# Optimization experiments

Measured on AMD Instinct MI355X. Metric: run time of the kernel, lower is better.

Reference implementation:

```python
import jax, jax.numpy as jnp
import numpy as np

N_NODES = 100000
N_EDGES = 3200000
N_FEAT = 16
N_GRAPHS = 1024


def setup_inputs() -> dict:
    key = jax.random.key(0)
    ks = jax.random.split(key, 12)
    x = jax.random.normal(ks[0], (N_NODES, N_FEAT), dtype=jnp.float32)
    edge_index = jax.random.randint(ks[1], (2, N_EDGES), 0, N_NODES, dtype=jnp.int32)
    batch = jnp.sort(jax.random.randint(ks[2], (N_NODES,), 0, N_GRAPHS, dtype=jnp.int32))
    def lin(k, fan_in, fan_out):
        s = 1.0 / np.sqrt(fan_in)
        return jax.random.uniform(k, (fan_in, fan_out), jnp.float32, -s, s)
    W1 = lin(ks[3], N_FEAT, 64); b1 = jnp.zeros((64,), jnp.float32)
    W2 = lin(ks[4], 64, 32);     b2 = jnp.zeros((32,), jnp.float32)
    fc1_W = lin(ks[5], 32, 16);  fc1_b = jnp.zeros((16,), jnp.float32)
    fc2_W = lin(ks[6], 16, 1);   fc2_b = jnp.zeros((1,), jnp.float32)
    return {"x": x, "edge_index": edge_index, "batch": batch,
            "W1": W1, "b1": b1, "W2": W2, "b2": b2,
            "fc1_W": fc1_W, "fc1_b": fc1_b, "fc2_W": fc2_W, "fc2_b": fc2_b}


def _gcn_conv(h, W, b, src, dst, norm, n_nodes):
    # h: [N, Fin] -> [N, Fout]; symmetric-normalized scatter-add (PyG GCNConv)
    h = h @ W
    msg = h[src] * norm[:, None]            # edge-wise gather + scale
    out = jax.ops.segment_sum(msg, dst, num_segments=n_nodes)
    return out + b


def reference(x, edge_index, batch, W1, b1, W2, b2, fc1_W, fc1_b, fc2_W, fc2_b):
    n_nodes = x.shape[0]
    # add self-loops
    loops = jnp.arange(n_nodes, dtype=edge_index.dtype)
    src = jnp.concatenate([edge_index[0], loops])
    dst = jnp.concatenate([edge_index[1], loops])
    deg = jax.ops.segment_sum(jnp.ones_like(dst, dtype=x.dtype), dst, num_segments=n_nodes)
    dinv = jnp.where(deg > 0, jax.lax.rsqrt(deg), 0.0)
    norm = dinv[src] * dinv[dst]

    h = jax.nn.relu(_gcn_conv(x, W1, b1, src, dst, norm, n_nodes))
    # dropout p=0.2 is identity at inference
    h = jax.nn.relu(_gcn_conv(h, W2, b2, src, dst, norm, n_nodes))

    # global mean pool over graphs
    sums = jax.ops.segment_sum(h, batch, num_segments=N_GRAPHS)
    cnts = jax.ops.segment_sum(jnp.ones((n_nodes,), h.dtype), batch, num_segments=N_GRAPHS)
    g = sums / jnp.maximum(cnts, 1.0)[:, None]

    g = jax.nn.relu(g @ fc1_W + fc1_b)
    # dropout p=0.5 is identity at inference
    out = g @ fc2_W + fc2_b
    return jax.nn.sigmoid(out)  # [N_GRAPHS, 1]
```

## Files before the change

kernel.cpp:

```cpp
#include <hip/hip_runtime.h>
#include <math.h>

#define NNODES  100000
#define NEDGES  3200000
#define NGRAPHS 1024
#define BNODES  196
#define NBUCK   ((NNODES + BNODES - 1) / BNODES)
#define SCAP    12288
#define SLDS    7168
#define CHUNK   4096
#define NCHUNKS ((NEDGES + CHUNK - 1) / CHUNK)

typedef int iv4 __attribute__((ext_vector_type(4)));
typedef float fv2 __attribute__((ext_vector_type(2)));

#if defined(__has_builtin)
#if __has_builtin(__builtin_amdgcn_cvt_pk_f32_fp8) && __has_builtin(__builtin_amdgcn_cvt_pk_fp8_f32)
#define HW_FP8 1
#endif
#endif

__device__ __forceinline__ unsigned bf16pair(float a, float b) {
    unsigned ua = __float_as_uint(a), ub = __float_as_uint(b);
    ua += 0x7fffu + ((ua >> 16) & 1u);
    ub += 0x7fffu + ((ub >> 16) & 1u);
    return (ua >> 16) | (ub & 0xffff0000u);
}
__device__ __forceinline__ float bflo(unsigned u) { return __uint_as_float(u << 16); }
__device__ __forceinline__ float bfhi(unsigned u) { return __uint_as_float(u & 0xffff0000u); }

__device__ __forceinline__ unsigned fp8_of(float v) {
    unsigned s = (__float_as_uint(v) >> 24) & 0x80u;
    float a = fminf(fabsf(v), 448.f);
    unsigned ub = __float_as_uint(a);
    unsigned lsb = (ub >> 20) & 1u;
    ub += 0x0007FFFFu + lsb;
    int em = (int)(ub >> 20) - (120 << 3);
    if (em < 1) return s;
    if (em > 0x7E) em = 0x7E;
    return s | (unsigned)em;
}
__device__ __forceinline__ float fp8_to_f(unsigned b) {
    unsigned em = b & 0x7Fu;
    unsigned s = (b & 0x80u) << 24;
    float f = __uint_as_float(s | ((em + 0x3C0u) << 20));
    return (em >= 8u) ? f : 0.f;
}
__device__ __forceinline__ unsigned fp8x4_pack(float a, float b, float c, float d) {
    a = fminf(fmaxf(a, -448.f), 448.f);
    b = fminf(fmaxf(b, -448.f), 448.f);
    c = fminf(fmaxf(c, -448.f), 448.f);
    d = fminf(fmaxf(d, -448.f), 448.f);
#ifdef HW_FP8
    int w = __builtin_amdgcn_cvt_pk_fp8_f32(a, b, 0, false);
    w = __builtin_amdgcn_cvt_pk_fp8_f32(c, d, w, true);
    return (unsigned)w;
#else
    return fp8_of(a) | (fp8_of(b) << 8) | (fp8_of(c) << 16) | (fp8_of(d) << 24);
#endif
}
__device__ __forceinline__ fv2 f8lo(unsigned w) {
#ifdef HW_FP8
    return __builtin_amdgcn_cvt_pk_f32_fp8((int)w, false);
#else
    fv2 t; t.x = fp8_to_f(w & 0xFFu); t.y = fp8_to_f((w >> 8) & 0xFFu); return t;
#endif
}
__device__ __forceinline__ fv2 f8hi(unsigned w) {
#ifdef HW_FP8
    return __builtin_amdgcn_cvt_pk_f32_fp8((int)w, true);
#else
    fv2 t; t.x = fp8_to_f((w >> 16) & 0xFFu); t.y = fp8_to_f(w >> 24); return t;
#endif
}


__global__ void zero4_kernel(int4* p, int nvec) {
    int i = blockIdx.x * blockDim.x + threadIdx.x;
    if (i < nvec) p[i] = make_int4(0, 0, 0, 0);
}


__global__ void binA_kernel(const int* __restrict__ src, const int* __restrict__ dst,
                            int* __restrict__ bucketCur, int* __restrict__ stage) {
    __shared__ int lcnt[NBUCK + 1];
    __shared__ int boff[NBUCK + 1];
    __shared__ int gbase[NBUCK + 1];
    __shared__ int cur[NBUCK + 1];
    __shared__ int wtot[4];
    __shared__ int packed[CHUNK];
    __shared__ unsigned short bof[CHUNK];
    int tid = threadIdx.x;
    int beg = blockIdx.x * CHUNK;
    int end = beg + CHUNK; if (end > NEDGES) end = NEDGES;
    int cnt = end - beg;

    for (int i = tid; i <= NBUCK; i += 256) lcnt[i] = 0;
    __syncthreads();

    int ent[16];
    int bk[16];
#pragma unroll
    for (int it = 0; it < 4; ++it) {
        int e0 = beg + tid * 4 + it * 1024;
        if (e0 < end) {
            iv4 d4 = __builtin_nontemporal_load((const iv4*)(dst + e0));
            iv4 s4 = __builtin_nontemporal_load((const iv4*)(src + e0));
            int b;
            b = d4.x / BNODES; ent[it*4+0] = s4.x | ((d4.x - b*BNODES) << 17); bk[it*4+0] = b; atomicAdd(&lcnt[b], 1);
            b = d4.y / BNODES; ent[it*4+1] = s4.y | ((d4.y - b*BNODES) << 17); bk[it*4+1] = b; atomicAdd(&lcnt[b], 1);
            b = d4.z / BNODES; ent[it*4+2] = s4.z | ((d4.z - b*BNODES) << 17); bk[it*4+2] = b; atomicAdd(&lcnt[b], 1);
            b = d4.w / BNODES; ent[it*4+3] = s4.w | ((d4.w - b*BNODES) << 17); bk[it*4+3] = b; atomicAdd(&lcnt[b], 1);
        } else {
            bk[it*4+0] = -1; bk[it*4+1] = -1; bk[it*4+2] = -1; bk[it*4+3] = -1;
            ent[it*4+0] = 0; ent[it*4+1] = 0; ent[it*4+2] = 0; ent[it*4+3] = 0;
        }
    }
    __syncthreads();

    int b0 = 2 * tid, b1 = 2 * tid + 1;
    int c0 = lcnt[b0];
    int c1 = (b1 < NBUCK) ? lcnt[b1] : 0;
    int sum = c0 + c1;
    int lane = tid & 63, wid = tid >> 6;
    int v = sum;
#pragma unroll
    for (int o = 1; o < 64; o <<= 1) {
        int t = __shfl_up(v, o, 64);
        if (lane >= o) v += t;
    }
    if (lane == 63) wtot[wid] = v;
    __syncthreads();
    int woff = 0;
#pragma unroll
    for (int w = 0; w < 4; ++w) woff += (w < wid) ? wtot[w] : 0;
    int excl = woff + v - sum;
    boff[b0] = excl; cur[b0] = excl;
    if (b1 < NBUCK) { boff[b1] = excl + c0; cur[b1] = excl + c0; }
    if (c0 > 0) gbase[b0] = atomicAdd(&bucketCur[b0], c0);
    if (b1 < NBUCK && c1 > 0) gbase[b1] = atomicAdd(&bucketCur[b1], c1);
    __syncthreads();

#pragma unroll
    for (int k = 0; k < 16; ++k) {
        int b = bk[k];
        if (b >= 0) {
            int p = atomicAdd(&cur[b], 1);
            packed[p] = ent[k];
            bof[p] = (unsigned short)b;
        }
    }
    __syncthreads();

    for (int i = tid; i < cnt; i += 256) {
        int b = bof[i];
        int addr = b * SCAP + gbase[b] + (i - boff[b]);
        stage[addr] = packed[i];
    }
}


__global__ void scanE_kernel(const int* __restrict__ bucketCur, int* __restrict__ ebase) {
    int lane = threadIdx.x;
    int run = 0;
    for (int base = 0; base < NBUCK; base += 64) {
        int idx = base + lane;
        int own = (idx < NBUCK) ? bucketCur[idx] : 0;
        int v = own;
        for (int o = 1; o < 64; o <<= 1) {
            int t = __shfl_up(v, o, 64);
            if (lane >= o) v += t;
        }
        if (idx < NBUCK) ebase[idx] = run + v - own;
        run += __shfl(v, 63, 64);
    }
}


__global__ void binB_kernel(const int* __restrict__ bucketCur, const int* __restrict__ ebase,
                            const int* __restrict__ stage, const float2* __restrict__ x,
                            int* __restrict__ entries, int* __restrict__ rowptr,
                            float* __restrict__ dinv, unsigned* __restrict__ xs) {
    __shared__ int s[256];
    __shared__ int ncur[256];
    __shared__ float ndinv[256];
    __shared__ int wt[4];
    __shared__ int se[SLDS];
    int b = blockIdx.x;
    int cntE = bucketCur[b];
    int eb = ebase[b];
    int nlo = b * BNODES;
    int nn = NNODES - nlo; if (nn > BNODES) nn = BNODES;
    int sb = b * SCAP;
    int tid = threadIdx.x;

    s[tid] = 0;
    __syncthreads();
    for (int e = tid; e < cntE; e += 256) {
        int w = stage[sb + e];
        if (e < SLDS) se[e] = w;
        atomicAdd(&s[(unsigned)w >> 17], 1);
    }
    __syncthreads();
    int v = s[tid];
    int lane = tid & 63, wid = tid >> 6;
    int iv = v;
#pragma unroll
    for (int o = 1; o < 64; o <<= 1) {
        int t = __shfl_up(iv, o, 64);
        if (lane >= o) iv += t;
    }
    if (lane == 63) wt[wid] = iv;
    __syncthreads();
    int woff = 0;
#pragma unroll
    for (int w2 = 0; w2 < 4; ++w2) woff += (w2 < wid) ? wt[w2] : 0;
    int excl = woff + iv - v;
    ncur[tid] = excl;
    if (tid < nn) {
        rowptr[nlo + tid] = eb + excl;
        float di = rsqrtf((float)(v + 1));
        dinv[nlo + tid] = di;
        ndinv[tid] = di;
    }
    if (b == NBUCK - 1 && tid == 0) rowptr[NNODES] = NEDGES;
    __syncthreads();
    for (int i = tid; i < nn * 8; i += 256) {
        int node = i >> 3, w = i & 7;
        float2 v2 = x[(size_t)(nlo + node) * 8 + w];
        float di = ndinv[node];
        xs[(nlo + node) * 8 + w] = bf16pair(v2.x * di, v2.y * di);
    }
    for (int e = tid; e < cntE; e += 256) {
        unsigned w = (unsigned)((e < SLDS) ? se[e] : stage[sb + e]);
        int dl = (int)(w >> 17);
        int slot = atomicAdd(&ncur[dl], 1);
        entries[eb + slot] = (int)(w & 0x1FFFFu);
    }
}


__device__ __forceinline__ void acc_bf(unsigned u, fv2& a) {
    fv2 t; t.x = bflo(u); t.y = bfhi(u);
    a += t;
}
#define ACCX4(V) { acc_bf((V).x, acc0); acc_bf((V).y, acc1); acc_bf((V).z, acc2); acc_bf((V).w, acc3); }
#define QRED(a) { a.x += __shfl_xor(a.x, 2); a.y += __shfl_xor(a.y, 2); \
                  a.x += __shfl_xor(a.x, 4); a.y += __shfl_xor(a.y, 4); }

__global__ void __launch_bounds__(256) gatherX_mlp_kernel(const int* __restrict__ entries,
        const int* __restrict__ rowptr, const float* __restrict__ dinv,
        const uint4* __restrict__ xsv,
        const float* __restrict__ W1, const float* __restrict__ b1,
        const float* __restrict__ W2, unsigned* __restrict__ hm2f) {
    __shared__ __align__(16) float w1s[16 * 64];
    __shared__ __align__(16) float w2s[64 * 32];
    __shared__ float bb1[64];
    int tid = threadIdx.x;
    for (int i = tid; i < 16 * 64; i += 256) w1s[i] = W1[i];
    for (int i = tid; i < 64 * 32; i += 256) w2s[i] = W2[i];
    if (tid < 64) bb1[tid] = b1[tid];
    __syncthreads();

    int t = blockIdx.x * 256 + tid;
    int n = t >> 3, lane = t & 7;
    int half = lane & 1, quad = lane >> 1;
    int beg = rowptr[n], end = rowptr[n + 1];
    fv2 acc0 = {0.f, 0.f}, acc1 = {0.f, 0.f}, acc2 = {0.f, 0.f}, acc3 = {0.f, 0.f};
    if (quad == 0) {
        uint4 sv = xsv[n * 2 + half];
        ACCX4(sv);
    }

    int nb = (end - beg) >> 4;
    const int* ep = entries + beg + (quad << 2);
    iv4 e = {0, 0, 0, 0};
    if (nb > 0) __builtin_memcpy(&e, ep, 16);
    for (int i = 1; i <= nb; ++i) {
        iv4 f = e;
        if (i < nb) __builtin_memcpy(&e, ep + (i << 4), 16);
        uint4 v0 = xsv[f.x * 2 + half];
        uint4 v1 = xsv[f.y * 2 + half];
        uint4 v2 = xsv[f.z * 2 + half];
        uint4 v3 = xsv[f.w * 2 + half];
        ACCX4(v0); ACCX4(v1); ACCX4(v2); ACCX4(v3);
    }
    int tp = beg + (nb << 4) + (quad << 2);
#pragma unroll
    for (int j = 0; j < 4; ++j) {
        if (tp + j < end) {
            int ee = entries[tp + j];
            uint4 v = xsv[ee * 2 + half];
            ACCX4(v);
        }
    }

    QRED(acc0); QRED(acc1); QRED(acc2); QRED(acc3);

    float di = dinv[n];
    float own[8];
    own[0] = acc0.x * di; own[1] = acc0.y * di; own[2] = acc1.x * di; own[3] = acc1.y * di;
    own[4] = acc2.x * di; own[5] = acc2.y * di; own[6] = acc3.x * di; own[7] = acc3.y * di;
    float oth[8];
#pragma unroll
    for (int i2 = 0; i2 < 8; ++i2) oth[i2] = __shfl_xor(own[i2], 1);
    float a16[16];
#pragma unroll
    for (int k = 0; k < 8; ++k) a16[k]     = (half == 0) ? own[k] : oth[k];
#pragma unroll
    for (int k = 0; k < 8; ++k) a16[8 + k] = (half == 0) ? oth[k] : own[k];

    float h[8];
    {
        int j0 = lane * 8;
#pragma unroll
        for (int jj = 0; jj < 8; ++jj) h[jj] = bb1[j0 + jj];
#pragma unroll
        for (int k = 0; k < 16; ++k) {
            const float4* wr = (const float4*)(w1s + k * 64 + j0);
            float4 wa = wr[0], wb = wr[1];
            float av = a16[k];
            h[0] += av * wa.x; h[1] += av * wa.y; h[2] += av * wa.z; h[3] += av * wa.w;
            h[4] += av * wb.x; h[5] += av * wb.y; h[6] += av * wb.z; h[7] += av * wb.w;
        }
#pragma unroll
        for (int jj = 0; jj < 8; ++jj) h[jj] = fmaxf(h[jj], 0.f);
    }

    {
        int j0c = lane * 4;
        float c0 = 0.f, c1 = 0.f, c2 = 0.f, c3 = 0.f;
#pragma unroll
        for (int k = 0; k < 64; ++k) {
            float hv = __shfl(h[k & 7], k >> 3, 8);
            float4 w = *(const float4*)(w2s + k * 32 + j0c);
            c0 += hv * w.x; c1 += hv * w.y; c2 += hv * w.z; c3 += hv * w.w;
        }
        float sc = di * 64.f;
        hm2f[n * 8 + lane] = fp8x4_pack(c0 * sc, c1 * sc, c2 * sc, c3 * sc);
    }
}


#define ACCH4(V) { q0lo += f8lo((V).x); q0hi += f8hi((V).x); \
                   q1lo += f8lo((V).y); q1hi += f8hi((V).y); \
                   q2lo += f8lo((V).z); q2hi += f8hi((V).z); \
                   q3lo += f8lo((V).w); q3hi += f8hi((V).w); }

__global__ void __launch_bounds__(256) gatherH_pool_kernel(const int* __restrict__ entries,
        const int* __restrict__ rowptr,
        const float* __restrict__ dinv, const uint4* __restrict__ hm4,
        const float4* __restrict__ b2, const int* __restrict__ batch,
        float* __restrict__ psum, float* __restrict__ pcnt) {
    __shared__ float lps[8][32];
    __shared__ float lpc[8];
    int tid = threadIdx.x;
    ((float*)lps)[tid] = 0.f;
    if (tid < 8) lpc[tid] = 0.f;
    __syncthreads();

    int t = blockIdx.x * 256 + tid;
    int n = t >> 3, lane = t & 7;
    int half = lane & 1, quad = lane >> 1;
    int g0 = batch[blockIdx.x * 32];
    int beg = rowptr[n], end = rowptr[n + 1];
    fv2 q0lo = {0.f,0.f}, q0hi = {0.f,0.f}, q1lo = {0.f,0.f}, q1hi = {0.f,0.f},
        q2lo = {0.f,0.f}, q2hi = {0.f,0.f}, q3lo = {0.f,0.f}, q3hi = {0.f,0.f};
    if (quad == 0) {
        uint4 sv = hm4[n * 2 + half];
        ACCH4(sv);
    }

    int nb = (end - beg) >> 4;
    const int* ep = entries + beg + (quad << 2);
    iv4 e = {0, 0, 0, 0};
    if (nb > 0) __builtin_memcpy(&e, ep, 16);
    for (int i = 1; i <= nb; ++i) {
        iv4 f = e;
        if (i < nb) __builtin_memcpy(&e, ep + (i << 4), 16);
        uint4 v0 = hm4[f.x * 2 + half];
        uint4 v1 = hm4[f.y * 2 + half];
        uint4 v2 = hm4[f.z * 2 + half];
        uint4 v3 = hm4[f.w * 2 + half];
        ACCH4(v0); ACCH4(v1); ACCH4(v2); ACCH4(v3);
    }
    int tp = beg + (nb << 4) + (quad << 2);
#pragma unroll
    for (int j = 0; j < 4; ++j) {
        if (tp + j < end) {
            int ee = entries[tp + j];
            uint4 v = hm4[ee * 2 + half];
            ACCH4(v);
        }
    }

    QRED(q0lo); QRED(q0hi); QRED(q1lo); QRED(q1hi);
    QRED(q2lo); QRED(q2hi); QRED(q3lo); QRED(q3hi);

    if (quad == 0) {
        float sc = dinv[n] * (1.0f / 64.f);
        float4 bv0 = b2[half * 4 + 0], bv1 = b2[half * 4 + 1],
               bv2 = b2[half * 4 + 2], bv3 = b2[half * 4 + 3];
        float vv[16];
        vv[0]  = fmaxf(q0lo.x * sc + bv0.x, 0.f);
        vv[1]  = fmaxf(q0lo.y * sc + bv0.y, 0.f);
        vv[2]  = fmaxf(q0hi.x * sc + bv0.z, 0.f);
        vv[3]  = fmaxf(q0hi.y * sc + bv0.w, 0.f);
        vv[4]  = fmaxf(q1lo.x * sc + bv1.x, 0.f);
        vv[5]  = fmaxf(q1lo.y * sc + bv1.y, 0.f);
        vv[6]  = fmaxf(q1hi.x * sc + bv1.z, 0.f);
        vv[7]  = fmaxf(q1hi.y * sc + bv1.w, 0.f);
        vv[8]  = fmaxf(q2lo.x * sc + bv2.x, 0.f);
        vv[9]  = fmaxf(q2lo.y * sc + bv2.y, 0.f);
        vv[10] = fmaxf(q2hi.x * sc + bv2.z, 0.f);
        vv[11] = fmaxf(q2hi.y * sc + bv2.w, 0.f);
        vv[12] = fmaxf(q3lo.x * sc + bv3.x, 0.f);
        vv[13] = fmaxf(q3lo.y * sc + bv3.y, 0.f);
        vv[14] = fmaxf(q3hi.x * sc + bv3.z, 0.f);
        vv[15] = fmaxf(q3hi.y * sc + bv3.w, 0.f);

        int g = batch[n], gr = g - g0;
        if (gr < 8) {
            float* pg = &lps[gr][half * 16];
#pragma unroll
            for (int k2 = 0; k2 < 16; ++k2) atomicAdd(pg + k2, vv[k2]);
            if (lane == 0) atomicAdd(&lpc[gr], 1.0f);
        } else {
            float* pg = psum + g * 32 + half * 16;
#pragma unroll
            for (int k2 = 0; k2 < 16; ++k2) atomicAdd(pg + k2, vv[k2]);
            if (lane == 0) atomicAdd(&pcnt[g], 1.0f);
        }
    }
    __syncthreads();
    int grf = tid >> 5, f = tid & 31;
    float v = lps[grf][f];
    if (v != 0.f) atomicAdd(&psum[(g0 + grf) * 32 + f], v);
    if (f == 0) {
        float c = lpc[grf];
        if (c != 0.f) atomicAdd(&pcnt[g0 + grf], c);
    }
}


__global__ void head_kernel(const float* __restrict__ psum, const float* __restrict__ pcnt,
                            const float* __restrict__ fc1W, const float* __restrict__ fc1b,
                            const float* __restrict__ fc2W, const float* __restrict__ fc2b,
                            float* __restrict__ out) {
    int g = blockIdx.x * blockDim.x + threadIdx.x;
    if (g >= NGRAPHS) return;
    float inv = 1.0f / fmaxf(pcnt[g], 1.0f);
    float gv[32];
#pragma unroll
    for (int k = 0; k < 32; ++k) gv[k] = psum[g * 32 + k] * inv;
    float o = fc2b[0];
#pragma unroll
    for (int j = 0; j < 16; ++j) {
        float h = fc1b[j];
#pragma unroll
        for (int k = 0; k < 32; ++k) h += gv[k] * fc1W[k * 16 + j];
        h = fmaxf(h, 0.f);
        o += h * fc2W[j];
    }
    out[g] = 1.0f / (1.0f + expf(-o));
}


extern "C" void kernel_launch(void* const* d_in, const int* in_sizes, int n_in,
                              void* d_out, int out_size, void* d_ws, size_t ws_size,
                              hipStream_t stream) {
    const float* x    = (const float*)d_in[0];
    const int*   ei   = (const int*)d_in[1];
    const int*   batch= (const int*)d_in[2];
    const float* W1   = (const float*)d_in[3];
    const float* b1   = (const float*)d_in[4];
    const float* W2   = (const float*)d_in[5];
    const float* b2   = (const float*)d_in[6];
    const float* fc1W = (const float*)d_in[7];
    const float* fc1b = (const float*)d_in[8];
    const float* fc2W = (const float*)d_in[9];
    const float* fc2b = (const float*)d_in[10];
    float* out = (float*)d_out;

    const int* src = ei;
    const int* dst = ei + NEDGES;

    char* wsb = (char*)d_ws;
    int*      bucketCur = (int*)wsb;
    float*    psum      = (float*)(wsb + 2048);
    float*    pcnt      = (float*)(wsb + 133120);
    int*      ebase     = (int*)(wsb + 137216);
    float*    dinv      = (float*)(wsb + 139264);
    int*      rowptr    = (int*)(wsb + 539264);
    int*      stage     = (int*)(wsb + 939392);
    int*      entries   = (int*)(wsb + 26056064);
    unsigned* xs        = (unsigned*)(wsb + 38856064);
    unsigned* hm2f      = (unsigned*)(wsb + 42056064);

    const int B = 256;
    zero4_kernel<<<(8576 + B - 1) / B, B, 0, stream>>>((int4*)wsb, 8576);

    binA_kernel<<<NCHUNKS, B, 0, stream>>>(src, dst, bucketCur, stage);
    scanE_kernel<<<1, 64, 0, stream>>>(bucketCur, ebase);
    binB_kernel<<<NBUCK, B, 0, stream>>>(bucketCur, ebase, stage, (const float2*)x,
                                         entries, rowptr, dinv, xs);

    const int GTH = NNODES * 8 / B;
    gatherX_mlp_kernel<<<GTH, B, 0, stream>>>(entries, rowptr, dinv,
                                              (const uint4*)xs, W1, b1, W2, hm2f);
    gatherH_pool_kernel<<<GTH, B, 0, stream>>>(entries, rowptr, dinv,
                                               (const uint4*)hm2f, (const float4*)b2,
                                               batch, psum, pcnt);
    head_kernel<<<(NGRAPHS + B - 1) / B, B, 0, stream>>>(psum, pcnt, fc1W, fc1b, fc2W, fc2b, out);
}
```

Measured before the change: 239.9 us.

## Pad CSR rows to multiples of 16 with dummy node, drop global scan

Each node's adjacency list is padded to a multiple of 16 using a dummy node index whose feature row is zeroed. Buckets get fixed-size regions in the CSR array, so the separate exclusive-scan kernel goes away and a rowend array is stored. The gather loops lose their scalar tail handling and are software-pipelined so the next group's feature loads are issued before the current group is accumulated. The cost is extra padded gathers (about 7.5 per node on average), a dummy row that every padded slot hits, and a smaller per-bucket staging capacity (SCAP 8192), which assumes no bucket exceeds it for these inputs.

```diff
diff --git a/kernel.cpp b/kernel.cpp
--- a/kernel.cpp
+++ b/kernel.cpp
@@ -6,8 +6,10 @@
 #define NGRAPHS 1024
 #define BNODES  196
 #define NBUCK   ((NNODES + BNODES - 1) / BNODES)
-#define SCAP    12288
+#define SCAP    8192
+#define PADCAP  10240
 #define SLDS    7168
+#define DUMMY   NNODES
 #define CHUNK   4096
 #define NCHUNKS ((NEDGES + CHUNK - 1) / CHUNK)
 
@@ -160,26 +162,10 @@
 }
 
 
-__global__ void scanE_kernel(const int* __restrict__ bucketCur, int* __restrict__ ebase) {
-    int lane = threadIdx.x;
-    int run = 0;
-    for (int base = 0; base < NBUCK; base += 64) {
-        int idx = base + lane;
-        int own = (idx < NBUCK) ? bucketCur[idx] : 0;
-        int v = own;
-        for (int o = 1; o < 64; o <<= 1) {
-            int t = __shfl_up(v, o, 64);
-            if (lane >= o) v += t;
-        }
-        if (idx < NBUCK) ebase[idx] = run + v - own;
-        run += __shfl(v, 63, 64);
-    }
-}
-
-
-__global__ void binB_kernel(const int* __restrict__ bucketCur, const int* __restrict__ ebase,
+__global__ void binB_kernel(const int* __restrict__ bucketCur,
                             const int* __restrict__ stage, const float2* __restrict__ x,
                             int* __restrict__ entries, int* __restrict__ rowptr,
+                            int* __restrict__ rowend,
                             float* __restrict__ dinv, unsigned* __restrict__ xs) {
     __shared__ int s[256];
     __shared__ int ncur[256];
@@ -188,7 +174,7 @@
     __shared__ int se[SLDS];
     int b = blockIdx.x;
     int cntE = bucketCur[b];
-    int eb = ebase[b];
+    int bbase = b * PADCAP;
     int nlo = b * BNODES;
     int nn = NNODES - nlo; if (nn > BNODES) nn = BNODES;
     int sb = b * SCAP;
@@ -203,8 +189,9 @@
     }
     __syncthreads();
     int v = s[tid];
+    int p16 = (v + 15) & ~15;
     int lane = tid & 63, wid = tid >> 6;
-    int iv = v;
+    int iv = p16;
 #pragma unroll
     for (int o = 1; o < 64; o <<= 1) {
         int t = __shfl_up(iv, o, 64);
@@ -215,15 +202,15 @@
     int woff = 0;
 #pragma unroll
     for (int w2 = 0; w2 < 4; ++w2) woff += (w2 < wid) ? wt[w2] : 0;
-    int excl = woff + iv - v;
-    ncur[tid] = excl;
+    int pexcl = woff + iv - p16;
+    ncur[tid] = pexcl;
     if (tid < nn) {
-        rowptr[nlo + tid] = eb + excl;
+        rowptr[nlo + tid] = bbase + pexcl;
+        rowend[nlo + tid] = bbase + pexcl + p16;
         float di = rsqrtf((float)(v + 1));
         dinv[nlo + tid] = di;
         ndinv[tid] = di;
     }
-    if (b == NBUCK - 1 && tid == 0) rowptr[NNODES] = NEDGES;
     __syncthreads();
     for (int i = tid; i < nn * 8; i += 256) {
         int node = i >> 3, w = i & 7;
@@ -231,11 +218,18 @@
         float di = ndinv[node];
         xs[(nlo + node) * 8 + w] = bf16pair(v2.x * di, v2.y * di);
     }
+    if (b == NBUCK - 1) {
+        for (int i = tid; i < 8; i += 256) xs[NNODES * 8 + i] = 0u;
+    }
+    if (tid < nn) {
+        int base = bbase + pexcl;
+        for (int j = v; j < p16; ++j) entries[base + j] = DUMMY;
+    }
     for (int e = tid; e < cntE; e += 256) {
         unsigned w = (unsigned)((e < SLDS) ? se[e] : stage[sb + e]);
         int dl = (int)(w >> 17);
         int slot = atomicAdd(&ncur[dl], 1);
-        entries[eb + slot] = (int)(w & 0x1FFFFu);
+        entries[bbase + slot] = (int)(w & 0x1FFFFu);
     }
 }
 
@@ -249,8 +243,8 @@
                   a.x += __shfl_xor(a.x, 4); a.y += __shfl_xor(a.y, 4); }
 
 __global__ void __launch_bounds__(256) gatherX_mlp_kernel(const int* __restrict__ entries,
-        const int* __restrict__ rowptr, const float* __restrict__ dinv,
-        const uint4* __restrict__ xsv,
+        const int* __restrict__ rowptr, const int* __restrict__ rowend,
+        const float* __restrict__ dinv, const uint4* __restrict__ xsv,
         const float* __restrict__ W1, const float* __restrict__ b1,
         const float* __restrict__ W2, unsigned* __restrict__ hm2f) {
     __shared__ __align__(16) float w1s[16 * 64];
@@ -260,39 +254,38 @@
     for (int i = tid; i < 16 * 64; i += 256) w1s[i] = W1[i];
     for (int i = tid; i < 64 * 32; i += 256) w2s[i] = W2[i];
     if (tid < 64) bb1[tid] = b1[tid];
+    if (blockIdx.x == 0 && tid < 8) hm2f[NNODES * 8 + tid] = 0u;
     __syncthreads();
 
     int t = blockIdx.x * 256 + tid;
     int n = t >> 3, lane = t & 7;
     int half = lane & 1, quad = lane >> 1;
-    int beg = rowptr[n], end = rowptr[n + 1];
+    int beg = rowptr[n];
+    int nb = (rowend[n] - beg) >> 4;
     fv2 acc0 = {0.f, 0.f}, acc1 = {0.f, 0.f}, acc2 = {0.f, 0.f}, acc3 = {0.f, 0.f};
     if (quad == 0) {
         uint4 sv = xsv[n * 2 + half];
         ACCX4(sv);
     }
 
-    int nb = (end - beg) >> 4;
     const int* ep = entries + beg + (quad << 2);
-    iv4 e = {0, 0, 0, 0};
-    if (nb > 0) __builtin_memcpy(&e, ep, 16);
-    for (int i = 1; i <= nb; ++i) {
-        iv4 f = e;
-        if (i < nb) __builtin_memcpy(&e, ep + (i << 4), 16);
-        uint4 v0 = xsv[f.x * 2 + half];
-        uint4 v1 = xsv[f.y * 2 + half];
-        uint4 v2 = xsv[f.z * 2 + half];
-        uint4 v3 = xsv[f.w * 2 + half];
-        ACCX4(v0); ACCX4(v1); ACCX4(v2); ACCX4(v3);
-    }
-    int tp = beg + (nb << 4) + (quad << 2);
-#pragma unroll
-    for (int j = 0; j < 4; ++j) {
-        if (tp + j < end) {
-            int ee = entries[tp + j];
-            uint4 v = xsv[ee * 2 + half];
-            ACCX4(v);
-        }
+    if (nb > 0) {
+        uint4 p0, p1, p2, p3;
+        iv4 enx = {0, 0, 0, 0};
+        {
+            iv4 e; __builtin_memcpy(&e, ep, 16);
+            p0 = xsv[e.x * 2 + half]; p1 = xsv[e.y * 2 + half];
+            p2 = xsv[e.z * 2 + half]; p3 = xsv[e.w * 2 + half];
+            if (nb > 1) __builtin_memcpy(&enx, ep + 16, 16);
+        }
+        for (int i = 1; i < nb; ++i) {
+            uint4 c0 = xsv[enx.x * 2 + half], c1 = xsv[enx.y * 2 + half],
+                  c2 = xsv[enx.z * 2 + half], c3 = xsv[enx.w * 2 + half];
+            if (i + 1 < nb) __builtin_memcpy(&enx, ep + ((i + 1) << 4), 16);
+            ACCX4(p0); ACCX4(p1); ACCX4(p2); ACCX4(p3);
+            p0 = c0; p1 = c1; p2 = c2; p3 = c3;
+        }
+        ACCX4(p0); ACCX4(p1); ACCX4(p2); ACCX4(p3);
     }
 
     QRED(acc0); QRED(acc1); QRED(acc2); QRED(acc3);
@@ -348,7 +341,7 @@
                    q3lo += f8lo((V).w); q3hi += f8hi((V).w); }
 
 __global__ void __launch_bounds__(256) gatherH_pool_kernel(const int* __restrict__ entries,
-        const int* __restrict__ rowptr,
+        const int* __restrict__ rowptr, const int* __restrict__ rowend,
         const float* __restrict__ dinv, const uint4* __restrict__ hm4,
         const float4* __restrict__ b2, const int* __restrict__ batch,
         float* __restrict__ psum, float* __restrict__ pcnt) {
@@ -363,7 +356,8 @@
     int n = t >> 3, lane = t & 7;
     int half = lane & 1, quad = lane >> 1;
     int g0 = batch[blockIdx.x * 32];
-    int beg = rowptr[n], end = rowptr[n + 1];
+    int beg = rowptr[n];
+    int nb = (rowend[n] - beg) >> 4;
     fv2 q0lo = {0.f,0.f}, q0hi = {0.f,0.f}, q1lo = {0.f,0.f}, q1hi = {0.f,0.f},
         q2lo = {0.f,0.f}, q2hi = {0.f,0.f}, q3lo = {0.f,0.f}, q3hi = {0.f,0.f};
     if (quad == 0) {
@@ -371,27 +365,24 @@
         ACCH4(sv);
     }
 
-    int nb = (end - beg) >> 4;
     const int* ep = entries + beg + (quad << 2);
-    iv4 e = {0, 0, 0, 0};
-    if (nb > 0) __builtin_memcpy(&e, ep, 16);
-    for (int i = 1; i <= nb; ++i) {
-        iv4 f = e;
-        if (i < nb) __builtin_memcpy(&e, ep + (i << 4), 16);
-        uint4 v0 = hm4[f.x * 2 + half];
-        uint4 v1 = hm4[f.y * 2 + half];
-        uint4 v2 = hm4[f.z * 2 + half];
-        uint4 v3 = hm4[f.w * 2 + half];
-        ACCH4(v0); ACCH4(v1); ACCH4(v2); ACCH4(v3);
-    }
-    int tp = beg + (nb << 4) + (quad << 2);
-#pragma unroll
-    for (int j = 0; j < 4; ++j) {
-        if (tp + j < end) {
-            int ee = entries[tp + j];
-            uint4 v = hm4[ee * 2 + half];
-            ACCH4(v);
-        }
+    if (nb > 0) {
+        uint4 p0, p1, p2, p3;
+        iv4 enx = {0, 0, 0, 0};
+        {
+            iv4 e; __builtin_memcpy(&e, ep, 16);
+            p0 = hm4[e.x * 2 + half]; p1 = hm4[e.y * 2 + half];
+            p2 = hm4[e.z * 2 + half]; p3 = hm4[e.w * 2 + half];
+            if (nb > 1) __builtin_memcpy(&enx, ep + 16, 16);
+        }
+        for (int i = 1; i < nb; ++i) {
+            uint4 c0 = hm4[enx.x * 2 + half], c1 = hm4[enx.y * 2 + half],
+                  c2 = hm4[enx.z * 2 + half], c3 = hm4[enx.w * 2 + half];
+            if (i + 1 < nb) __builtin_memcpy(&enx, ep + ((i + 1) << 4), 16);
+            ACCH4(p0); ACCH4(p1); ACCH4(p2); ACCH4(p3);
+            p0 = c0; p1 = c1; p2 = c2; p3 = c3;
+        }
+        ACCH4(p0); ACCH4(p1); ACCH4(p2); ACCH4(p3);
     }
 
     QRED(q0lo); QRED(q0hi); QRED(q1lo); QRED(q1hi);
@@ -489,26 +480,25 @@
     int*      bucketCur = (int*)wsb;
     float*    psum      = (float*)(wsb + 2048);
     float*    pcnt      = (float*)(wsb + 133120);
-    int*      ebase     = (int*)(wsb + 137216);
-    float*    dinv      = (float*)(wsb + 139264);
-    int*      rowptr    = (int*)(wsb + 539264);
-    int*      stage     = (int*)(wsb + 939392);
-    int*      entries   = (int*)(wsb + 26056064);
-    unsigned* xs        = (unsigned*)(wsb + 38856064);
-    unsigned* hm2f      = (unsigned*)(wsb + 42056064);
+    float*    dinv      = (float*)(wsb + 137216);
+    int*      rowptr    = (int*)(wsb + 537216);
+    int*      rowend    = (int*)(wsb + 937216);
+    int*      stage     = (int*)(wsb + 1337216);
+    int*      entries   = (int*)(wsb + 18081664);
+    unsigned* xs        = (unsigned*)(wsb + 39012224);
+    unsigned* hm2f      = (unsigned*)(wsb + 42212256);
 
     const int B = 256;
     zero4_kernel<<<(8576 + B - 1) / B, B, 0, stream>>>((int4*)wsb, 8576);
 
     binA_kernel<<<NCHUNKS, B, 0, stream>>>(src, dst, bucketCur, stage);
-    scanE_kernel<<<1, 64, 0, stream>>>(bucketCur, ebase);
-    binB_kernel<<<NBUCK, B, 0, stream>>>(bucketCur, ebase, stage, (const float2*)x,
-                                         entries, rowptr, dinv, xs);
+    binB_kernel<<<NBUCK, B, 0, stream>>>(bucketCur, stage, (const float2*)x,
+                                         entries, rowptr, rowend, dinv, xs);
 
     const int GTH = NNODES * 8 / B;
-    gatherX_mlp_kernel<<<GTH, B, 0, stream>>>(entries, rowptr, dinv,
+    gatherX_mlp_kernel<<<GTH, B, 0, stream>>>(entries, rowptr, rowend, dinv,
                                               (const uint4*)xs, W1, b1, W2, hm2f);
-    gatherH_pool_kernel<<<GTH, B, 0, stream>>>(entries, rowptr, dinv,
+    gatherH_pool_kernel<<<GTH, B, 0, stream>>>(entries, rowptr, rowend, dinv,
                                                (const uint4*)hm2f, (const float4*)b2,
                                                batch, psum, pcnt);
     head_kernel<<<(NGRAPHS + B - 1) / B, B, 0, stream>>>(psum, pcnt, fc1W, fc1b, fc2W, fc2b, out);
```

Result: faster. 231.0 us (-3.7%).
